# Kernel tuning notes

Measured on AMD Instinct MI355X. Metric: run time of the kernel, lower is better.

The kernel has to match this reference:

```python
import jax, jax.numpy as jnp
import numpy as np

B, S, D, T = 8, 4096, 512, 8  # batch, seq (dim), d_model, nheads


def _sinusoidal_pe(dim, d_model):
    # matches torch: pe[:,0::2]=sin(pos*div), pe[:,1::2]=cos(pos*div)
    pos = jnp.arange(dim, dtype=jnp.float32)[:, None]
    div = jnp.exp(jnp.arange(0, d_model, 2, dtype=jnp.float32) * (-(np.log(10000.0) / d_model)))
    ang = pos * div  # [dim, d_model//2]
    return jnp.stack([jnp.sin(ang), jnp.cos(ang)], axis=-1).reshape(dim, d_model)


def setup_inputs() -> dict:
    key = jax.random.key(0)
    ks = jax.random.split(key, 7)
    sc = 1.0 / np.sqrt(D)
    return {
        "x": jax.random.normal(ks[0], (B, S, D), dtype=jnp.float32),
        "Wk": jax.random.normal(ks[1], (T, D, D), dtype=jnp.float32) * sc,
        "bk": jax.random.normal(ks[2], (T, D), dtype=jnp.float32) * sc,
        "Wq": jax.random.normal(ks[3], (T, D, D), dtype=jnp.float32) * sc,
        "bq": jax.random.normal(ks[4], (T, D), dtype=jnp.float32) * sc,
        "Wv": jax.random.normal(ks[5], (T, D, D), dtype=jnp.float32) * sc,
        "bv": jax.random.normal(ks[6], (T, D), dtype=jnp.float32) * sc,
    }


def reference(x, Wk, bk, Wq, bq, Wv, bv):
    b, s, d = x.shape
    t = Wk.shape[0]
    c = s // t  # head chunk length
    x = x + _sinusoidal_pe(s, d)[None]  # PE add
    xh = x.reshape(b, t, c, d)  # 'b (t c) d -> b t c d'
    # torch Linear: y = x @ W^T + b ; W is [out, in]
    k = jnp.einsum('btcd,ted->btce', xh, Wk) + bk[None, :, None, :]
    q = jnp.einsum('btcd,ted->btce', xh, Wq) + bq[None, :, None, :]
    v = jnp.einsum('btcd,ted->btce', xh, Wv) + bv[None, :, None, :]
    # note: k @ q^T (not q @ k^T) and divide by d_model (not sqrt) -- faithful
    scores = jnp.einsum('btid,btjd->btij', k, q) * (1.0 / d)
    attn = jax.nn.softmax(scores, axis=-1)
    out = jnp.einsum('btij,btjd->btid', attn, v)
    return out.reshape(b, s, d)  # concat heads along seq dim
```

## Files before the change

kernel.cpp:

```cpp
#include <hip/hip_runtime.h>
#include <hip/hip_bf16.h>
#include <cstdint>
#include <cstddef>


typedef __bf16 bf16_t;
typedef __bf16 bf16x4 __attribute__((ext_vector_type(4)));
typedef __bf16 bf16x8 __attribute__((ext_vector_type(8)));
typedef float  f32x4  __attribute__((ext_vector_type(4)));

#define GAS __attribute__((address_space(1)))
#define LAS __attribute__((address_space(3)))

__global__ __launch_bounds__(256) void prep_kernel(
    const float* __restrict__ x, bf16_t* __restrict__ xpe,
    const float* __restrict__ w0, const float* __restrict__ w1,
    const float* __restrict__ w2, bf16_t* __restrict__ o0,
    bf16_t* __restrict__ o1, bf16_t* __restrict__ o2)
{
    if (blockIdx.x < 2048) {
        const float cexp = -0.017988946039015984f;
        int i = blockIdx.x * 256 + threadIdx.x;
        int d4 = i & 127;
        int s  = i >> 7;
        int d  = d4 * 4;
        float fs = (float)s;
        float a0 = fs * __expf(cexp * (float)d);
        float a1 = fs * __expf(cexp * (float)(d + 2));
        float s0, c0, s1, c1;
        sincosf(a0, &s0, &c0);
        sincosf(a1, &s1, &c1);
        size_t base = (size_t)s * 512 + d;
        #pragma unroll
        for (int b = 0; b < 8; ++b) {
            float4 xv = *(const float4*)(x + (size_t)b * 2097152 + base);
            bf16x4 o;
            o[0] = (bf16_t)(xv.x + s0);
            o[1] = (bf16_t)(xv.y + c0);
            o[2] = (bf16_t)(xv.z + s1);
            o[3] = (bf16_t)(xv.w + c1);
            *(bf16x4*)(xpe + (size_t)b * 2097152 + base) = o;
        }
    } else {
        const int per = 524288;
        for (int i = (blockIdx.x - 2048) * 256 + threadIdx.x; i < 3 * per;
             i += 1024 * 256) {
            int f = i / per, off = i - f * per;
            const float* s = f == 0 ? w0 : (f == 1 ? w1 : w2);
            bf16_t*      o = f == 0 ? o0 : (f == 1 ? o1 : o2);
            float4 v = ((const float4*)s)[off];
            bf16x4 r;
            r[0] = (bf16_t)v.x; r[1] = (bf16_t)v.y;
            r[2] = (bf16_t)v.z; r[3] = (bf16_t)v.w;
            ((bf16x4*)o)[off] = r;
        }
    }
}

template<int BIAS_MODE, int OUT_BF16>
__global__ __launch_bounds__(256, 2) void gemm_nt(
    const bf16_t* __restrict__ A, const bf16_t* __restrict__ Bm,
    void* __restrict__ C, const float* __restrict__ bias,
    long aStr, long bStr, long cStr, int aByT, int bByT, float scale)
{
    constexpr int LD = 512;
    int L  = blockIdx.y * 16 + blockIdx.x;
    int t  = L & 7;
    int b  = (L >> 3) & 7;
    int tile = L >> 6;
    int bt = (b << 3) | t;
    const bf16_t* Ab = A  + (size_t)(aByT ? t : bt) * aStr;
    const bf16_t* Bb = Bm + (size_t)(bByT ? t : bt) * bStr;
    int ti = (tile >> 2) << 7;
    int tn = (tile & 3) << 7;

    __shared__ __align__(1024) char lds[65536];

    const int tid  = threadIdx.x;
    const int l    = tid & 63;
    const int w    = tid >> 6;
    const int lrow = l >> 3;
    const int hd   = (l & 7) ^ lrow;
    const int wrow = w >> 1, wcol = w & 1;
    const int rA   = l & 15;
    const int hb   = l >> 4;
    const int x7   = l & 7;

    f32x4 acc[4][4] = {};

    auto stage = [&](int buf, int k0) {
        char* ldsA = lds + buf * 32768;
        char* ldsB = ldsA + 16384;
        #pragma unroll
        for (int p = 0; p < 4; ++p) {
            int c    = w * 4 + p;
            int grow = c * 8 + lrow;
            const bf16_t* srcA = Ab + (size_t)(ti + grow) * LD + k0 + hd * 8;
            const bf16_t* srcB = Bb + (size_t)(tn + grow) * LD + k0 + hd * 8;
            __builtin_amdgcn_global_load_lds((GAS void*)srcA, (LAS void*)(ldsA + c * 1024 + l * 16), 16, 0, 0);
            __builtin_amdgcn_global_load_lds((GAS void*)srcB, (LAS void*)(ldsB + c * 1024 + l * 16), 16, 0, 0);
        }
    };

    stage(0, 0);
    __syncthreads();
    for (int it = 0; it < 8; ++it) {
        if (it < 7) stage((it + 1) & 1, (it + 1) * 64);
        const char* ldsA = lds + (it & 1) * 32768;
        const char* ldsB = ldsA + 16384;
        #pragma unroll
        for (int kk = 0; kk < 2; ++kk) {
            bf16x8 a[4], bb[4];
            #pragma unroll
            for (int m = 0; m < 4; ++m) {
                int off = (wrow * 64 + m * 16 + rA) * 128 + (((kk << 2) | hb) ^ x7) * 16;
                a[m] = *(const bf16x8*)(ldsA + off);
            }
            #pragma unroll
            for (int n = 0; n < 4; ++n) {
                int off = (wcol * 64 + n * 16 + rA) * 128 + (((kk << 2) | hb) ^ x7) * 16;
                bb[n] = *(const bf16x8*)(ldsB + off);
            }
            #pragma unroll
            for (int m = 0; m < 4; ++m)
                #pragma unroll
                for (int n = 0; n < 4; ++n)
                    acc[m][n] = __builtin_amdgcn_mfma_f32_16x16x32_bf16(a[m], bb[n], acc[m][n], 0, 0, 0);
        }
        __syncthreads();
    }

    const float* biasT = bias ? bias + t * 512 : bias;
    int r0 = ti + wrow * 64;
    int c0 = tn + wcol * 64;
    #pragma unroll
    for (int m = 0; m < 4; ++m)
        #pragma unroll
        for (int n = 0; n < 4; ++n) {
            int col = c0 + n * 16 + rA;
            float bc = (BIAS_MODE == 1) ? biasT[col] : 0.0f;
            f32x4 v = acc[m][n];
            #pragma unroll
            for (int r = 0; r < 4; ++r) {
                int row = r0 + m * 16 + hb * 4 + r;
                float val = v[r] * scale + ((BIAS_MODE == 2) ? biasT[row] : bc);
                size_t off = (size_t)bt * cStr + (size_t)row * LD + col;
                if (OUT_BF16) ((bf16_t*)C)[off] = (bf16_t)val;
                else          ((float*)C)[off]  = val;
            }
        }
}

__global__ __launch_bounds__(512) void attn_fused(
    const bf16_t* __restrict__ K, const bf16_t* __restrict__ Q,
    const bf16_t* __restrict__ VT, float* __restrict__ Out)
{
    int L  = blockIdx.x;
    int bt = ((L >> 6) << 3) | (L & 7);
    int ti = ((L >> 3) & 7) << 6;
    const bf16_t* Kb = K  + (size_t)bt * 262144;
    const bf16_t* Qb = Q  + (size_t)bt * 262144;
    const bf16_t* Vb = VT + (size_t)bt * 262144;

    __shared__ __align__(1024) char smem[143360];
    char* Pl = smem + 73728;
    float* smax_p = (float*)(smem + 139264);
    float* ssum_p = (float*)(smem + 141312);

    const int tid = threadIdx.x;
    const int l   = tid & 63;
    const int wv  = tid >> 6;
    const int rA  = l & 15;
    const int hb  = l >> 4;
    const int key = (rA >> 1) & 3;

    const int srow = tid >> 2;
    const int sslot = tid & 3;

    f32x4 acc[4][4] = {};

    auto stageKQ = [&](int buf, int d0) {
        char* kA = smem + buf * 4096;
        char* qB = smem + 8192 + buf * 32768;
        if (tid < 256) {
            const bf16_t* src = Kb + (size_t)(ti + srow) * 512 + d0 +
                                (sslot ^ ((srow >> 1) & 3)) * 8;
            __builtin_amdgcn_global_load_lds((GAS void*)src, (LAS void*)(kA + tid * 16), 16, 0, 0);
        }
        #pragma unroll
        for (int u = 0; u < 4; ++u) {
            int q2 = u * 512 + tid;
            int row = q2 >> 2, slot = q2 & 3;
            const bf16_t* src = Qb + (size_t)row * 512 + d0 +
                                (slot ^ ((row >> 1) & 3)) * 8;
            __builtin_amdgcn_global_load_lds((GAS void*)src, (LAS void*)(qB + q2 * 16), 16, 0, 0);
        }
    };

    stageKQ(0, 0);
    __syncthreads();
    for (int it = 0; it < 16; ++it) {
        if (it < 15) stageKQ((it + 1) & 1, (it + 1) * 32);
        const char* kA = smem + (it & 1) * 4096;
        const char* qB = smem + 8192 + (it & 1) * 32768;
        bf16x8 a[4], b[4];
        #pragma unroll
        for (int m = 0; m < 4; ++m)
            a[m] = *(const bf16x8*)(kA + (m * 16 + rA) * 64 + ((hb ^ key) << 4));
        #pragma unroll
        for (int n = 0; n < 4; ++n) {
            int j = wv * 64 + n * 16 + rA;
            b[n] = *(const bf16x8*)(qB + j * 64 + ((hb ^ key) << 4));
        }
        #pragma unroll
        for (int m = 0; m < 4; ++m)
            #pragma unroll
            for (int n = 0; n < 4; ++n)
                acc[m][n] = __builtin_amdgcn_mfma_f32_16x16x32_bf16(a[m], b[n], acc[m][n], 0, 0, 0);
        __syncthreads();
    }

    float red[4][4];
    #pragma unroll
    for (int m = 0; m < 4; ++m)
        #pragma unroll
        for (int r = 0; r < 4; ++r) {
            float mx = acc[m][0][r];
            #pragma unroll
            for (int n = 1; n < 4; ++n) mx = fmaxf(mx, acc[m][n][r]);
            #pragma unroll
            for (int o = 1; o < 16; o <<= 1) mx = fmaxf(mx, __shfl_xor(mx, o, 64));
            red[m][r] = mx;
        }
    if (rA < 4) {
        #pragma unroll
        for (int m = 0; m < 4; ++m)
            smax_p[(m * 16 + hb * 4 + rA) * 8 + wv] = red[m][rA];
    }
    __syncthreads();
    float rstat[4][4];
    #pragma unroll
    for (int m = 0; m < 4; ++m)
        #pragma unroll
        for (int r = 0; r < 4; ++r) {
            int row = m * 16 + hb * 4 + r;
            f32x4 p0 = *(const f32x4*)(smax_p + row * 8);
            f32x4 p1 = *(const f32x4*)(smax_p + row * 8 + 4);
            rstat[m][r] = fmaxf(fmaxf(fmaxf(p0[0], p0[1]), fmaxf(p0[2], p0[3])),
                                fmaxf(fmaxf(p1[0], p1[1]), fmaxf(p1[2], p1[3])));
        }
    const float inv512 = 1.0f / 512.0f;
    #pragma unroll
    for (int m = 0; m < 4; ++m)
        #pragma unroll
        for (int r = 0; r < 4; ++r) {
            float sum = 0.0f;
            #pragma unroll
            for (int n = 0; n < 4; ++n) {
                float e = __expf((acc[m][n][r] - rstat[m][r]) * inv512);
                acc[m][n][r] = e;
                sum += e;
            }
            #pragma unroll
            for (int o = 1; o < 16; o <<= 1) sum += __shfl_xor(sum, o, 64);
            red[m][r] = sum;
        }
    if (rA < 4) {
        #pragma unroll
        for (int m = 0; m < 4; ++m)
            ssum_p[(m * 16 + hb * 4 + rA) * 8 + wv] = red[m][rA];
    }
    __syncthreads();
    #pragma unroll
    for (int m = 0; m < 4; ++m)
        #pragma unroll
        for (int r = 0; r < 4; ++r) {
            int row = m * 16 + hb * 4 + r;
            f32x4 p0 = *(const f32x4*)(ssum_p + row * 8);
            f32x4 p1 = *(const f32x4*)(ssum_p + row * 8 + 4);
            rstat[m][r] = 1.0f / (((p0[0] + p0[1]) + (p0[2] + p0[3])) +
                                  ((p1[0] + p1[1]) + (p1[2] + p1[3])));
        }

    #pragma unroll
    for (int m = 0; m < 4; ++m)
        #pragma unroll
        for (int n = 0; n < 4; ++n) {
            int j = wv * 64 + n * 16 + rA;
            int jslot = j >> 3, jrem = (j & 7) * 2;
            #pragma unroll
            for (int r = 0; r < 4; ++r) {
                int i = m * 16 + hb * 4 + r;
                *(bf16_t*)(Pl + i * 1024 + ((jslot ^ (i & 7)) << 4) + jrem) =
                    (bf16_t)(acc[m][n][r] * rstat[m][r]);
            }
        }
    __syncthreads();

    auto stageV = [&](int buf, int j0) {
        char* vB = smem + 8192 + buf * 32768;
        #pragma unroll
        for (int u = 0; u < 4; ++u) {
            int q2 = u * 512 + tid;
            int e = q2 >> 2, slot = q2 & 3;
            const bf16_t* src = Vb + (size_t)e * 512 + j0 +
                                (slot ^ ((e >> 1) & 3)) * 8;
            __builtin_amdgcn_global_load_lds((GAS void*)src, (LAS void*)(vB + q2 * 16), 16, 0, 0);
        }
    };

    f32x4 acc2[4][4] = {};
    stageV(0, 0);
    __syncthreads();
    for (int it = 0; it < 16; ++it) {
        if (it < 15) stageV((it + 1) & 1, (it + 1) * 32);
        const char* vB = smem + 8192 + (it & 1) * 32768;
        int jcb = it * 4;
        bf16x8 a[4], b[4];
        #pragma unroll
        for (int m = 0; m < 4; ++m) {
            int i = m * 16 + rA;
            a[m] = *(const bf16x8*)(Pl + i * 1024 + (((jcb + hb) ^ (i & 7)) << 4));
        }
        #pragma unroll
        for (int n = 0; n < 4; ++n) {
            int e = wv * 64 + n * 16 + rA;
            b[n] = *(const bf16x8*)(vB + e * 64 + ((hb ^ key) << 4));
        }
        #pragma unroll
        for (int m = 0; m < 4; ++m)
            #pragma unroll
            for (int n = 0; n < 4; ++n)
                acc2[m][n] = __builtin_amdgcn_mfma_f32_16x16x32_bf16(a[m], b[n], acc2[m][n], 0, 0, 0);
        __syncthreads();
    }

    #pragma unroll
    for (int m = 0; m < 4; ++m)
        #pragma unroll
        for (int n = 0; n < 4; ++n) {
            int e = wv * 64 + n * 16 + rA;
            #pragma unroll
            for (int r = 0; r < 4; ++r) {
                int i = ti + m * 16 + hb * 4 + r;
                Out[(size_t)bt * 262144 + (size_t)i * 512 + e] = acc2[m][n][r];
            }
        }
}

extern "C" void kernel_launch(void* const* d_in, const int* in_sizes, int n_in,
                              void* d_out, int out_size, void* d_ws, size_t ws_size,
                              hipStream_t stream)
{
    const float* x  = (const float*)d_in[0];
    const float* Wk = (const float*)d_in[1];
    const float* bk = (const float*)d_in[2];
    const float* Wq = (const float*)d_in[3];
    const float* bq = (const float*)d_in[4];
    const float* Wv = (const float*)d_in[5];
    const float* bv = (const float*)d_in[6];
    float* out = (float*)d_out;
    char*  ws  = (char*)d_ws;

    bf16_t* k    = (bf16_t*)(ws + 0);
    bf16_t* q    = (bf16_t*)(ws + 33554432);
    bf16_t* vt   = (bf16_t*)(ws + 67108864);
    bf16_t* xpe  = (bf16_t*)(ws + 100663296);
    bf16_t* wkb  = (bf16_t*)(ws + 134217728);
    bf16_t* wqb  = (bf16_t*)(ws + 138412032);
    bf16_t* wvb  = (bf16_t*)(ws + 142606336);

    const long S2 = 262144;

    prep_kernel<<<3072, 256, 0, stream>>>(x, xpe, Wk, Wq, Wv, wkb, wqb, wvb);

    dim3 gg(16, 64);
    gemm_nt<1, 1><<<gg, 256, 0, stream>>>(xpe, wkb, k, bk, S2, S2, S2, 0, 1, 1.0f);
    gemm_nt<1, 1><<<gg, 256, 0, stream>>>(xpe, wqb, q, bq, S2, S2, S2, 0, 1, 1.0f);
    gemm_nt<2, 1><<<gg, 256, 0, stream>>>(wvb, xpe, vt, bv, S2, S2, S2, 1, 0, 1.0f);
    attn_fused<<<512, 512, 0, stream>>>(k, q, vt, out);
}
```

Before: 284.7 us.

## Use 16 waves per attention block and remap GEMM block-to-tile order

The attention kernel doubles its block size to 1024 threads (16 waves), so each wave covers 32 columns instead of 64. The per-row max and sum reductions are rewritten for 16 wave partials, and the staging loops are split across more threads. Separately, the GEMM block index is remapped so that consecutive blocks work on tiles of the same batch-head, which should improve L2 reuse of A/B panels. More waves per block can hide more latency but raise LDS use and synchronisation cost, and only one block still fits per CU.

Result: slower. 303.3 us (+6.5%).

```diff
diff --git a/kernel.cpp b/kernel.cpp
--- a/kernel.cpp
+++ b/kernel.cpp
@@ -65,10 +65,10 @@
 {
     constexpr int LD = 512;
     int L  = blockIdx.y * 16 + blockIdx.x;
-    int t  = L & 7;
-    int b  = (L >> 3) & 7;
-    int tile = L >> 6;
-    int bt = (b << 3) | t;
+    int wk = (L & 7) * 128 + (L >> 3);
+    int bt = wk >> 4;
+    int tile = wk & 15;
+    int t  = bt & 7;
     const bf16_t* Ab = A  + (size_t)(aByT ? t : bt) * aStr;
     const bf16_t* Bb = Bm + (size_t)(bByT ? t : bt) * bStr;
     int ti = (tile >> 2) << 7;
@@ -151,7 +151,7 @@
         }
 }
 
-__global__ __launch_bounds__(512) void attn_fused(
+__global__ __launch_bounds__(1024) void attn_fused(
     const bf16_t* __restrict__ K, const bf16_t* __restrict__ Q,
     const bf16_t* __restrict__ VT, float* __restrict__ Out)
 {
@@ -162,10 +162,10 @@
     const bf16_t* Qb = Q  + (size_t)bt * 262144;
     const bf16_t* Vb = VT + (size_t)bt * 262144;
 
-    __shared__ __align__(1024) char smem[143360];
+    __shared__ __align__(1024) char smem[147456];
     char* Pl = smem + 73728;
     float* smax_p = (float*)(smem + 139264);
-    float* ssum_p = (float*)(smem + 141312);
+    float* ssum_p = (float*)(smem + 143360);
 
     const int tid = threadIdx.x;
     const int l   = tid & 63;
@@ -174,22 +174,20 @@
     const int hb  = l >> 4;
     const int key = (rA >> 1) & 3;
 
-    const int srow = tid >> 2;
-    const int sslot = tid & 3;
-
-    f32x4 acc[4][4] = {};
+    f32x4 acc[4][2] = {};
 
     auto stageKQ = [&](int buf, int d0) {
         char* kA = smem + buf * 4096;
         char* qB = smem + 8192 + buf * 32768;
         if (tid < 256) {
-            const bf16_t* src = Kb + (size_t)(ti + srow) * 512 + d0 +
-                                (sslot ^ ((srow >> 1) & 3)) * 8;
+            int row = tid >> 2, slot = tid & 3;
+            const bf16_t* src = Kb + (size_t)(ti + row) * 512 + d0 +
+                                (slot ^ ((row >> 1) & 3)) * 8;
             __builtin_amdgcn_global_load_lds((GAS void*)src, (LAS void*)(kA + tid * 16), 16, 0, 0);
         }
         #pragma unroll
-        for (int u = 0; u < 4; ++u) {
-            int q2 = u * 512 + tid;
+        for (int u = 0; u < 2; ++u) {
+            int q2 = u * 1024 + tid;
             int row = q2 >> 2, slot = q2 & 3;
             const bf16_t* src = Qb + (size_t)row * 512 + d0 +
                                 (slot ^ ((row >> 1) & 3)) * 8;
@@ -203,19 +201,19 @@
         if (it < 15) stageKQ((it + 1) & 1, (it + 1) * 32);
         const char* kA = smem + (it & 1) * 4096;
         const char* qB = smem + 8192 + (it & 1) * 32768;
-        bf16x8 a[4], b[4];
+        bf16x8 a[4], b[2];
         #pragma unroll
         for (int m = 0; m < 4; ++m)
             a[m] = *(const bf16x8*)(kA + (m * 16 + rA) * 64 + ((hb ^ key) << 4));
         #pragma unroll
-        for (int n = 0; n < 4; ++n) {
-            int j = wv * 64 + n * 16 + rA;
+        for (int n = 0; n < 2; ++n) {
+            int j = wv * 32 + n * 16 + rA;
             b[n] = *(const bf16x8*)(qB + j * 64 + ((hb ^ key) << 4));
         }
         #pragma unroll
         for (int m = 0; m < 4; ++m)
             #pragma unroll
-            for (int n = 0; n < 4; ++n)
+            for (int n = 0; n < 2; ++n)
                 acc[m][n] = __builtin_amdgcn_mfma_f32_16x16x32_bf16(a[m], b[n], acc[m][n], 0, 0, 0);
         __syncthreads();
     }
@@ -225,9 +223,7 @@
     for (int m = 0; m < 4; ++m)
         #pragma unroll
         for (int r = 0; r < 4; ++r) {
-            float mx = acc[m][0][r];
-            #pragma unroll
-            for (int n = 1; n < 4; ++n) mx = fmaxf(mx, acc[m][n][r]);
+            float mx = fmaxf(acc[m][0][r], acc[m][1][r]);
             #pragma unroll
             for (int o = 1; o < 16; o <<= 1) mx = fmaxf(mx, __shfl_xor(mx, o, 64));
             red[m][r] = mx;
@@ -235,7 +231,7 @@
     if (rA < 4) {
         #pragma unroll
         for (int m = 0; m < 4; ++m)
-            smax_p[(m * 16 + hb * 4 + rA) * 8 + wv] = red[m][rA];
+            smax_p[(m * 16 + hb * 4 + rA) * 16 + wv] = red[m][rA];
     }
     __syncthreads();
     float rstat[4][4];
@@ -244,23 +240,23 @@
         #pragma unroll
         for (int r = 0; r < 4; ++r) {
             int row = m * 16 + hb * 4 + r;
-            f32x4 p0 = *(const f32x4*)(smax_p + row * 8);
-            f32x4 p1 = *(const f32x4*)(smax_p + row * 8 + 4);
-            rstat[m][r] = fmaxf(fmaxf(fmaxf(p0[0], p0[1]), fmaxf(p0[2], p0[3])),
-                                fmaxf(fmaxf(p1[0], p1[1]), fmaxf(p1[2], p1[3])));
+            float mx = -1e30f;
+            #pragma unroll
+            for (int u = 0; u < 4; ++u) {
+                f32x4 p = *(const f32x4*)(smax_p + row * 16 + u * 4);
+                mx = fmaxf(mx, fmaxf(fmaxf(p[0], p[1]), fmaxf(p[2], p[3])));
+            }
+            rstat[m][r] = mx;
         }
     const float inv512 = 1.0f / 512.0f;
     #pragma unroll
     for (int m = 0; m < 4; ++m)
         #pragma unroll
         for (int r = 0; r < 4; ++r) {
-            float sum = 0.0f;
-            #pragma unroll
-            for (int n = 0; n < 4; ++n) {
-                float e = __expf((acc[m][n][r] - rstat[m][r]) * inv512);
-                acc[m][n][r] = e;
-                sum += e;
-            }
+            float e0 = __expf((acc[m][0][r] - rstat[m][r]) * inv512);
+            float e1 = __expf((acc[m][1][r] - rstat[m][r]) * inv512);
+            acc[m][0][r] = e0; acc[m][1][r] = e1;
+            float sum = e0 + e1;
             #pragma unroll
             for (int o = 1; o < 16; o <<= 1) sum += __shfl_xor(sum, o, 64);
             red[m][r] = sum;
@@ -268,7 +264,7 @@
     if (rA < 4) {
         #pragma unroll
         for (int m = 0; m < 4; ++m)
-            ssum_p[(m * 16 + hb * 4 + rA) * 8 + wv] = red[m][rA];
+            ssum_p[(m * 16 + hb * 4 + rA) * 16 + wv] = red[m][rA];
     }
     __syncthreads();
     #pragma unroll
@@ -276,17 +272,20 @@
         #pragma unroll
         for (int r = 0; r < 4; ++r) {
             int row = m * 16 + hb * 4 + r;
-            f32x4 p0 = *(const f32x4*)(ssum_p + row * 8);
-            f32x4 p1 = *(const f32x4*)(ssum_p + row * 8 + 4);
-            rstat[m][r] = 1.0f / (((p0[0] + p0[1]) + (p0[2] + p0[3])) +
-                                  ((p1[0] + p1[1]) + (p1[2] + p1[3])));
-        }
-
-    #pragma unroll
-    for (int m = 0; m < 4; ++m)
-        #pragma unroll
-        for (int n = 0; n < 4; ++n) {
-            int j = wv * 64 + n * 16 + rA;
+            float s = 0.0f;
+            #pragma unroll
+            for (int u = 0; u < 4; ++u) {
+                f32x4 p = *(const f32x4*)(ssum_p + row * 16 + u * 4);
+                s += ((p[0] + p[1]) + (p[2] + p[3]));
+            }
+            rstat[m][r] = 1.0f / s;
+        }
+
+    #pragma unroll
+    for (int m = 0; m < 4; ++m)
+        #pragma unroll
+        for (int n = 0; n < 2; ++n) {
+            int j = wv * 32 + n * 16 + rA;
             int jslot = j >> 3, jrem = (j & 7) * 2;
             #pragma unroll
             for (int r = 0; r < 4; ++r) {
@@ -300,8 +299,8 @@
     auto stageV = [&](int buf, int j0) {
         char* vB = smem + 8192 + buf * 32768;
         #pragma unroll
-        for (int u = 0; u < 4; ++u) {
-            int q2 = u * 512 + tid;
+        for (int u = 0; u < 2; ++u) {
+            int q2 = u * 1024 + tid;
             int e = q2 >> 2, slot = q2 & 3;
             const bf16_t* src = Vb + (size_t)e * 512 + j0 +
                                 (slot ^ ((e >> 1) & 3)) * 8;
@@ -309,28 +308,28 @@
         }
     };
 
-    f32x4 acc2[4][4] = {};
+    f32x4 acc2[4][2] = {};
     stageV(0, 0);
     __syncthreads();
     for (int it = 0; it < 16; ++it) {
         if (it < 15) stageV((it + 1) & 1, (it + 1) * 32);
         const char* vB = smem + 8192 + (it & 1) * 32768;
         int jcb = it * 4;
-        bf16x8 a[4], b[4];
+        bf16x8 a[4], b[2];
         #pragma unroll
         for (int m = 0; m < 4; ++m) {
             int i = m * 16 + rA;
             a[m] = *(const bf16x8*)(Pl + i * 1024 + (((jcb + hb) ^ (i & 7)) << 4));
         }
         #pragma unroll
-        for (int n = 0; n < 4; ++n) {
-            int e = wv * 64 + n * 16 + rA;
+        for (int n = 0; n < 2; ++n) {
+            int e = wv * 32 + n * 16 + rA;
             b[n] = *(const bf16x8*)(vB + e * 64 + ((hb ^ key) << 4));
         }
         #pragma unroll
         for (int m = 0; m < 4; ++m)
             #pragma unroll
-            for (int n = 0; n < 4; ++n)
+            for (int n = 0; n < 2; ++n)
                 acc2[m][n] = __builtin_amdgcn_mfma_f32_16x16x32_bf16(a[m], b[n], acc2[m][n], 0, 0, 0);
         __syncthreads();
     }
@@ -338,8 +337,8 @@
     #pragma unroll
     for (int m = 0; m < 4; ++m)
         #pragma unroll
-        for (int n = 0; n < 4; ++n) {
-            int e = wv * 64 + n * 16 + rA;
+        for (int n = 0; n < 2; ++n) {
+            int e = wv * 32 + n * 16 + rA;
             #pragma unroll
             for (int r = 0; r < 4; ++r) {
                 int i = ti + m * 16 + hb * 4 + r;
@@ -378,5 +377,5 @@
     gemm_nt<1, 1><<<gg, 256, 0, stream>>>(xpe, wkb, k, bk, S2, S2, S2, 0, 1, 1.0f);
     gemm_nt<1, 1><<<gg, 256, 0, stream>>>(xpe, wqb, q, bq, S2, S2, S2, 0, 1, 1.0f);
     gemm_nt<2, 1><<<gg, 256, 0, stream>>>(wvb, xpe, vt, bv, S2, S2, S2, 1, 0, 1.0f);
-    attn_fused<<<512, 512, 0, stream>>>(k, q, vt, out);
+    attn_fused<<<512, 1024, 0, stream>>>(k, q, vt, out);
 }
```
